# Performance work log

Hardware: AMD Instinct MI355X
Metric: run time of the kernel (lower is better)

Reference implementation:

```python
import jax, jax.numpy as jnp
import numpy as np

WIN = 11      # window_size
SIGMA = 1.5
CH = 1        # channel
LEVELS = 5
C1 = 0.01 ** 2
C2 = 0.03 ** 2
MS_WEIGHTS = np.array([0.0448, 0.2856, 0.3001, 0.2363, 0.1333], dtype=np.float32)


def _gaussian_window(dtype):
    x = jnp.arange(WIN, dtype=jnp.float32) - WIN // 2
    g = jnp.exp(-(x ** 2) / (2.0 * SIGMA ** 2))
    g = g / g.sum()
    w2 = jnp.outer(g, g)  # [K, K]
    # depthwise kernel [C, 1, K, K]
    return jnp.broadcast_to(w2[None, None], (CH, 1, WIN, WIN)).astype(dtype)


def _blur(x, w):
    # depthwise 11x11 Gaussian blur, SAME padding (= pad window_size//2)
    return jax.lax.conv_general_dilated(
        x, w, window_strides=(1, 1), padding='SAME',
        dimension_numbers=('NCHW', 'OIHW', 'NCHW'),
        feature_group_count=CH)


def _ssim_level(img1, img2, w):
    mu1 = _blur(img1, w)
    mu2 = _blur(img2, w)
    mu1_sq = mu1 * mu1
    mu2_sq = mu2 * mu2
    mu1_mu2 = mu1 * mu2
    sigma1_sq = _blur(img1 * img1, w) - mu1_sq
    sigma2_sq = _blur(img2 * img2, w) - mu2_sq
    sigma12 = _blur(img1 * img2, w) - mu1_mu2
    denom_c = sigma1_sq + sigma2_sq + C2
    mcs_map = (2.0 * sigma12 + C2) / denom_c
    ssim_map = ((2.0 * mu1_mu2 + C1) / (mu1_sq + mu2_sq + C1)) * mcs_map
    return ssim_map.mean(), mcs_map.mean()


def _avg_pool2(x):
    B, C, H, W = x.shape
    return x.reshape(B, C, H // 2, 2, W // 2, 2).mean(axis=(3, 5))


def reference(img1, img2):
    w = _gaussian_window(img1.dtype)
    weights = jnp.asarray(MS_WEIGHTS, dtype=img1.dtype)
    mssim, mcs = [], []
    for _ in range(LEVELS):  # small fixed loop over pyramid levels
        s, m = _ssim_level(img1, img2, w)
        mssim.append(s)
        mcs.append(m)
        img1 = _avg_pool2(img1)
        img2 = _avg_pool2(img2)
    mssim = jnp.stack(mssim)
    mcs = jnp.stack(mcs)
    return jnp.prod(mcs[:LEVELS - 1] ** weights[:LEVELS - 1]) * mssim[LEVELS - 1] ** weights[LEVELS - 1]


def setup_inputs() -> dict:
    key = jax.random.key(0)
    k1, k2 = jax.random.split(key)
    img1 = jax.random.uniform(k1, (32, 1, 512, 512), dtype=jnp.float32)
    # correlated second image so ssim/mcs means stay positive (fractional powers)
    img2 = jnp.clip(img1 + 0.1 * jax.random.normal(k2, img1.shape, dtype=jnp.float32), 0.0, 1.0)
    return {"img1": img1, "img2": img2}
```

## Files before the change

### kernel.cpp

```cpp
#include <hip/hip_runtime.h>
#include <math.h>


typedef float v2f __attribute__((ext_vector_type(2)));

#define TILE 32
#define HALO 5
#define SROWS 42
#define SMEM_FLOATS 5384

struct GaussW { float w[11]; };

#define C1_ (0.01f * 0.01f)
#define C2_ (0.03f * 0.03f)

__device__ __forceinline__ void ssim_tile(
        const float* __restrict__ p1, const float* __restrict__ p2,
        int W, int tile_x, int tile_y, const GaussW& gw,
        float2* __restrict__ resslot, float* smem, int tid) {
    v2f* hbSD = (v2f*)smem;
    v2f* hbSQ = (v2f*)(smem + 2 * SROWS * TILE);
    float* red = smem + 4 * SROWS * TILE;

    const bool xfast = (tile_x >= 8) && (tile_x + TILE + 8 <= W);

    for (int it = tid; it < SROWS * 8; it += 256) {
        int r = it >> 3, c4 = it & 7;
        int gy = tile_y + r - HALO;
        int gx0 = tile_x + (c4 << 2) - 8;
        bool rowok = (gy >= 0) && (gy < W);
        const float* row1 = p1 + (size_t)gy * W;
        const float* row2 = p2 + (size_t)gy * W;
        float a1[20], a2[20];
#pragma unroll
        for (int i = 0; i < 20; i++) { a1[i] = 0.f; a2[i] = 0.f; }
        if (xfast) {
            if (rowok) {
#pragma unroll
                for (int q = 0; q < 5; q++) {
                    float4 v1 = *(const float4*)(row1 + gx0 + q * 4);
                    float4 v2v = *(const float4*)(row2 + gx0 + q * 4);
                    a1[q*4+0] = v1.x;  a1[q*4+1] = v1.y;  a1[q*4+2] = v1.z;  a1[q*4+3] = v1.w;
                    a2[q*4+0] = v2v.x; a2[q*4+1] = v2v.y; a2[q*4+2] = v2v.z; a2[q*4+3] = v2v.w;
                }
            }
        } else {
#pragma unroll
            for (int q = 0; q < 5; q++) {
                int g = gx0 + q * 4;
                if (rowok && g >= 0 && g + 4 <= W) {
                    float4 v1 = *(const float4*)(row1 + g);
                    float4 v2v = *(const float4*)(row2 + g);
                    a1[q*4+0] = v1.x;  a1[q*4+1] = v1.y;  a1[q*4+2] = v1.z;  a1[q*4+3] = v1.w;
                    a2[q*4+0] = v2v.x; a2[q*4+1] = v2v.y; a2[q*4+2] = v2v.z; a2[q*4+3] = v2v.w;
                }
            }
        }
        v2f SD[14], SQ[14];
#pragma unroll
        for (int i = 0; i < 14; i++) {
            float x = a1[i + 3], y = a2[i + 3];
            v2f sd = {x + y, x - y};
            SD[i] = sd;
            SQ[i] = sd * sd;
        }
        v2f hsd[4] = {(v2f)(0.f), (v2f)(0.f), (v2f)(0.f), (v2f)(0.f)};
        v2f hsq[4] = {(v2f)(0.f), (v2f)(0.f), (v2f)(0.f), (v2f)(0.f)};
#pragma unroll
        for (int k = 0; k < 11; k++) {
            float wk = gw.w[k];
#pragma unroll
            for (int j = 0; j < 4; j++) {
                hsd[j] += wk * SD[j + k];
                hsq[j] += wk * SQ[j + k];
            }
        }
        int ob = r * TILE + (c4 << 2);
#pragma unroll
        for (int j = 0; j < 4; j++) { hbSD[ob + j] = hsd[j]; hbSQ[ob + j] = hsq[j]; }
    }
    __syncthreads();

    float ssim_v = 0.f, mcs_v = 0.f;
    {
        int tx = tid & 31, y0 = (tid >> 5) * 4;
        v2f msd[4], msq[4];
        {
            v2f v[14];
#pragma unroll
            for (int r = 0; r < 14; r++) v[r] = hbSD[(y0 + r) * TILE + tx];
#pragma unroll
            for (int j = 0; j < 4; j++) {
                v2f s = (v2f)(0.f);
#pragma unroll
                for (int k = 0; k < 11; k++) s += gw.w[k] * v[j + k];
                msd[j] = s;
            }
        }
        {
            v2f v[14];
#pragma unroll
            for (int r = 0; r < 14; r++) v[r] = hbSQ[(y0 + r) * TILE + tx];
#pragma unroll
            for (int j = 0; j < 4; j++) {
                v2f s = (v2f)(0.f);
#pragma unroll
                for (int k = 0; k < 11; k++) s += gw.w[k] * v[j + k];
                msq[j] = s;
            }
        }
#pragma unroll
        for (int j = 0; j < 4; j++) {
            float bs = msd[j].x, bd = msd[j].y;
            float bs2 = msq[j].x, bd2 = msq[j].y;
            float qp = bs * bs, qm = bd * bd;
            float u = bs2 - qp;
            float v = bd2 - qm;
            float mcs  = (0.5f * (u - v) + C2_) / (0.5f * (u + v) + C2_);
            float ssim = ((0.5f * (qp - qm) + C1_) / (0.5f * (qp + qm) + C1_)) * mcs;
            ssim_v += ssim;
            mcs_v  += mcs;
        }
    }

#pragma unroll
    for (int off = 32; off > 0; off >>= 1) {
        ssim_v += __shfl_down(ssim_v, off);
        mcs_v  += __shfl_down(mcs_v, off);
    }
    int wave = tid >> 6, lane = tid & 63;
    if (lane == 0) { red[wave] = ssim_v; red[4 + wave] = mcs_v; }
    __syncthreads();
    if (tid == 0) {
        float S = red[0] + red[1] + red[2] + red[3];
        float M = red[4] + red[5] + red[6] + red[7];
        *resslot = make_float2(S, M);
    }
}

__device__ __forceinline__ void pyramid_region(
        const float* __restrict__ in1, const float* __restrict__ in2,
        int n, int reg,
        float* __restrict__ l1a, float* __restrict__ l1b,
        float* __restrict__ l2a, float* __restrict__ l2b,
        float* __restrict__ l3a, float* __restrict__ l3b,
        float* __restrict__ l4a, float* __restrict__ l4b,
        float* smem, int tid) {
    float* b1 = smem;
    float* b2 = smem + 1024;
    float* c1 = smem + 2048;
    float* c2 = smem + 2304;
    float* d1 = smem + 2560;
    float* d2 = smem + 2624;
    const int rx = reg & 7, ry = reg >> 3;
    const float* p1 = in1 + (size_t)n * 512 * 512;
    const float* p2 = in2 + (size_t)n * 512 * 512;

    for (int i = tid; i < 32 * 16; i += 256) {
        int oy = i >> 4, oxp = i & 15;
        int gy = ry * 64 + 2 * oy, gx = rx * 64 + 4 * oxp;
        float4 r10 = *(const float4*)(p1 + (size_t)gy * 512 + gx);
        float4 r11 = *(const float4*)(p1 + (size_t)(gy + 1) * 512 + gx);
        float4 r20 = *(const float4*)(p2 + (size_t)gy * 512 + gx);
        float4 r21 = *(const float4*)(p2 + (size_t)(gy + 1) * 512 + gx);
        float2 o1 = make_float2(0.25f * (r10.x + r10.y + r11.x + r11.y),
                                0.25f * (r10.z + r10.w + r11.z + r11.w));
        float2 o2 = make_float2(0.25f * (r20.x + r20.y + r21.x + r21.y),
                                0.25f * (r20.z + r20.w + r21.z + r21.w));
        *(float2*)&b1[oy * 32 + 2 * oxp] = o1;
        *(float2*)&b2[oy * 32 + 2 * oxp] = o2;
        size_t o = (size_t)n * 256 * 256 + (size_t)(ry * 32 + oy) * 256 + rx * 32 + 2 * oxp;
        *(float2*)&l1a[o] = o1;
        *(float2*)&l1b[o] = o2;
    }
    __syncthreads();
    if (tid < 16 * 8) {
        int oy = tid >> 3, oxp = tid & 7;
        float4 r10 = *(const float4*)&b1[(2 * oy) * 32 + 4 * oxp];
        float4 r11 = *(const float4*)&b1[(2 * oy + 1) * 32 + 4 * oxp];
        float4 r20 = *(const float4*)&b2[(2 * oy) * 32 + 4 * oxp];
        float4 r21 = *(const float4*)&b2[(2 * oy + 1) * 32 + 4 * oxp];
        float2 o1 = make_float2(0.25f * (r10.x + r10.y + r11.x + r11.y),
                                0.25f * (r10.z + r10.w + r11.z + r11.w));
        float2 o2 = make_float2(0.25f * (r20.x + r20.y + r21.x + r21.y),
                                0.25f * (r20.z + r20.w + r21.z + r21.w));
        *(float2*)&c1[oy * 16 + 2 * oxp] = o1;
        *(float2*)&c2[oy * 16 + 2 * oxp] = o2;
        size_t o = (size_t)n * 128 * 128 + (size_t)(ry * 16 + oy) * 128 + rx * 16 + 2 * oxp;
        *(float2*)&l2a[o] = o1;
        *(float2*)&l2b[o] = o2;
    }
    __syncthreads();
    if (tid < 8 * 4) {
        int oy = tid >> 2, oxp = tid & 3;
        float4 r10 = *(const float4*)&c1[(2 * oy) * 16 + 4 * oxp];
        float4 r11 = *(const float4*)&c1[(2 * oy + 1) * 16 + 4 * oxp];
        float4 r20 = *(const float4*)&c2[(2 * oy) * 16 + 4 * oxp];
        float4 r21 = *(const float4*)&c2[(2 * oy + 1) * 16 + 4 * oxp];
        float2 o1 = make_float2(0.25f * (r10.x + r10.y + r11.x + r11.y),
                                0.25f * (r10.z + r10.w + r11.z + r11.w));
        float2 o2 = make_float2(0.25f * (r20.x + r20.y + r21.x + r21.y),
                                0.25f * (r20.z + r20.w + r21.z + r21.w));
        *(float2*)&d1[oy * 8 + 2 * oxp] = o1;
        *(float2*)&d2[oy * 8 + 2 * oxp] = o2;
        size_t o = (size_t)n * 64 * 64 + (size_t)(ry * 8 + oy) * 64 + rx * 8 + 2 * oxp;
        *(float2*)&l3a[o] = o1;
        *(float2*)&l3b[o] = o2;
    }
    __syncthreads();
    if (tid < 4 * 2) {
        int oy = tid >> 1, oxp = tid & 1;
        float4 r10 = *(const float4*)&d1[(2 * oy) * 8 + 4 * oxp];
        float4 r11 = *(const float4*)&d1[(2 * oy + 1) * 8 + 4 * oxp];
        float4 r20 = *(const float4*)&d2[(2 * oy) * 8 + 4 * oxp];
        float4 r21 = *(const float4*)&d2[(2 * oy + 1) * 8 + 4 * oxp];
        float2 o1 = make_float2(0.25f * (r10.x + r10.y + r11.x + r11.y),
                                0.25f * (r10.z + r10.w + r11.z + r11.w));
        float2 o2 = make_float2(0.25f * (r20.x + r20.y + r21.x + r21.y),
                                0.25f * (r20.z + r20.w + r21.z + r21.w));
        size_t o = (size_t)n * 32 * 32 + (size_t)(ry * 4 + oy) * 32 + rx * 4 + 2 * oxp;
        *(float2*)&l4a[o] = o1;
        *(float2*)&l4b[o] = o2;
    }
}

__global__ __launch_bounds__(256, 7) void d1_kernel(
        const float* __restrict__ i0a, const float* __restrict__ i0b,
        float* __restrict__ l1a, float* __restrict__ l1b,
        float* __restrict__ l2a, float* __restrict__ l2b,
        float* __restrict__ l3a, float* __restrict__ l3b,
        float* __restrict__ l4a, float* __restrict__ l4b,
        float2* __restrict__ res0, GaussW gw) {
    __shared__ float smem[SMEM_FLOATS];
    const int tid = threadIdx.x;
    const int t = blockIdx.x;
    const int n = blockIdx.y;
    if (t < 64) {
        pyramid_region(i0a, i0b, n, t, l1a, l1b, l2a, l2b, l3a, l3b, l4a, l4b,
                       smem, tid);
    } else {
        int idx = t - 64;
        const float* p1 = i0a + (size_t)n * 512 * 512;
        const float* p2 = i0b + (size_t)n * 512 * 512;
        ssim_tile(p1, p2, 512, (idx & 15) << 5, (idx >> 4) << 5,
                  gw, &res0[n * 256 + idx], smem, tid);
    }
}

__global__ __launch_bounds__(256, 7) void d2_kernel(
        const float* __restrict__ l1a, const float* __restrict__ l1b,
        const float* __restrict__ l2a, const float* __restrict__ l2b,
        const float* __restrict__ l3a, const float* __restrict__ l3b,
        const float* __restrict__ l4a, const float* __restrict__ l4b,
        float2* __restrict__ res1, float2* __restrict__ res2,
        float2* __restrict__ res3, float2* __restrict__ res4, GaussW gw) {
    __shared__ float smem[SMEM_FLOATS];
    const int tid = threadIdx.x;
    const int t = blockIdx.x;
    const int n = blockIdx.y;
    const float* b1;
    const float* b2;
    int W, tx, ty;
    float2* slot;
    if (t < 64)      { W = 256; b1 = l1a; b2 = l1b; tx = (t & 7) << 5; ty = (t >> 3) << 5; slot = &res1[n * 64 + t]; }
    else if (t < 80) { int i = t - 64; W = 128; b1 = l2a; b2 = l2b; tx = (i & 3) << 5; ty = (i >> 2) << 5; slot = &res2[n * 16 + i]; }
    else if (t < 84) { int i = t - 80; W = 64; b1 = l3a; b2 = l3b; tx = (i & 1) << 5; ty = (i >> 1) << 5; slot = &res3[n * 4 + i]; }
    else             { W = 32; b1 = l4a; b2 = l4b; tx = 0; ty = 0; slot = &res4[n]; }
    ssim_tile(b1 + (size_t)n * W * W, b2 + (size_t)n * W * W, W,
              tx, ty, gw, slot, smem, tid);
}

__global__ void finalize_kernel(const float2* __restrict__ res0,
                                const float2* __restrict__ res1,
                                const float2* __restrict__ res2,
                                const float2* __restrict__ res3,
                                const float2* __restrict__ res4,
                                float* __restrict__ out, int N) {
    __shared__ float2 redf[5][4];
    const int tid = threadIdx.x;
    const float2* rr[5] = {res0, res1, res2, res3, res4};
    const int cnts[5] = {N * 256, N * 64, N * 16, N * 4, N};
#pragma unroll
    for (int l = 0; l < 5; l++) {
        float sx = 0.f, sy = 0.f;
        for (int i = tid; i < cnts[l]; i += 256) {
            float2 v = rr[l][i];
            sx += v.x;
            sy += v.y;
        }
#pragma unroll
        for (int off = 32; off > 0; off >>= 1) {
            sx += __shfl_down(sx, off);
            sy += __shfl_down(sy, off);
        }
        if ((tid & 63) == 0) redf[l][tid >> 6] = make_float2(sx, sy);
    }
    __syncthreads();
    if (tid == 0) {
        const float wts[5] = {0.0448f, 0.2856f, 0.3001f, 0.2363f, 0.1333f};
        float r = 1.f;
#pragma unroll
        for (int l = 0; l < 5; l++) {
            float sx = redf[l][0].x + redf[l][1].x + redf[l][2].x + redf[l][3].x;
            float sy = redf[l][0].y + redf[l][1].y + redf[l][2].y + redf[l][3].y;
            int Hl = 512 >> l;
            float cnt = (float)N * (float)Hl * (float)Hl;
            float ssim_m = sx / cnt;
            float mcs_m  = sy / cnt;
            if (l < 4) r *= powf(mcs_m, wts[l]);
            else       r *= powf(ssim_m, wts[4]);
        }
        out[0] = r;
    }
}

extern "C" void kernel_launch(void* const* d_in, const int* in_sizes, int n_in,
                              void* d_out, int out_size, void* d_ws, size_t ws_size,
                              hipStream_t stream) {
    const float* img1 = (const float*)d_in[0];
    const float* img2 = (const float*)d_in[1];
    float* out = (float*)d_out;
    const int HW0 = 512 * 512;
    const int N = in_sizes[0] / HW0;

    float* base = (float*)d_ws;
    size_t cur = 0;
    float* l1a = base + cur; cur += (size_t)N * 256 * 256;
    float* l1b = base + cur; cur += (size_t)N * 256 * 256;
    float* l2a = base + cur; cur += (size_t)N * 128 * 128;
    float* l2b = base + cur; cur += (size_t)N * 128 * 128;
    float* l3a = base + cur; cur += (size_t)N * 64 * 64;
    float* l3b = base + cur; cur += (size_t)N * 64 * 64;
    float* l4a = base + cur; cur += (size_t)N * 32 * 32;
    float* l4b = base + cur; cur += (size_t)N * 32 * 32;
    float2* res0 = (float2*)(base + cur); cur += (size_t)N * 512;
    float2* res1 = (float2*)(base + cur); cur += (size_t)N * 128;
    float2* res2 = (float2*)(base + cur); cur += (size_t)N * 32;
    float2* res3 = (float2*)(base + cur); cur += (size_t)N * 8;
    float2* res4 = (float2*)(base + cur); cur += (size_t)N * 2;

    GaussW gw;
    {
        double g[11], sum = 0.0;
        for (int i = 0; i < 11; i++) {
            double x = (double)(i - 5);
            g[i] = exp(-(x * x) / (2.0 * 1.5 * 1.5));
            sum += g[i];
        }
        for (int i = 0; i < 11; i++) gw.w[i] = (float)(g[i] / sum);
    }

    d1_kernel<<<dim3(320, N), 256, 0, stream>>>(
        img1, img2, l1a, l1b, l2a, l2b, l3a, l3b, l4a, l4b, res0, gw);
    d2_kernel<<<dim3(85, N), 256, 0, stream>>>(
        l1a, l1b, l2a, l2b, l3a, l3b, l4a, l4b, res1, res2, res3, res4, gw);
    finalize_kernel<<<1, 256, 0, stream>>>(res0, res1, res2, res3, res4, out, N);
}
```

Before: 156.0 us.

## Fuse pyramid downsampling into SSIM tile blocks using wave shuffles

Removes the 64 dedicated pyramid-building blocks per image. Each SSIM tile block now computes the 2x2 pooled pyramid levels 1-4 for its own 32x32 tile before the SSIM work. It uses a Morton-ordered thread mapping and wave-level shuffle reductions in place of shared-memory staging and block barriers. This cuts the grid from 320 to 256 blocks per image and reuses the tile's inputs, which are likely cached, for the pooling. The cost is extra uncoalesced float2 loads, and scattered small stores for the coarser levels.

Measured after the change: 162.1 us. +3.9%, slower.

```diff
diff --git a/kernel.cpp b/kernel.cpp
--- a/kernel.cpp
+++ b/kernel.cpp
@@ -138,92 +138,6 @@
     }
 }
 
-__device__ __forceinline__ void pyramid_region(
-        const float* __restrict__ in1, const float* __restrict__ in2,
-        int n, int reg,
-        float* __restrict__ l1a, float* __restrict__ l1b,
-        float* __restrict__ l2a, float* __restrict__ l2b,
-        float* __restrict__ l3a, float* __restrict__ l3b,
-        float* __restrict__ l4a, float* __restrict__ l4b,
-        float* smem, int tid) {
-    float* b1 = smem;
-    float* b2 = smem + 1024;
-    float* c1 = smem + 2048;
-    float* c2 = smem + 2304;
-    float* d1 = smem + 2560;
-    float* d2 = smem + 2624;
-    const int rx = reg & 7, ry = reg >> 3;
-    const float* p1 = in1 + (size_t)n * 512 * 512;
-    const float* p2 = in2 + (size_t)n * 512 * 512;
-
-    for (int i = tid; i < 32 * 16; i += 256) {
-        int oy = i >> 4, oxp = i & 15;
-        int gy = ry * 64 + 2 * oy, gx = rx * 64 + 4 * oxp;
-        float4 r10 = *(const float4*)(p1 + (size_t)gy * 512 + gx);
-        float4 r11 = *(const float4*)(p1 + (size_t)(gy + 1) * 512 + gx);
-        float4 r20 = *(const float4*)(p2 + (size_t)gy * 512 + gx);
-        float4 r21 = *(const float4*)(p2 + (size_t)(gy + 1) * 512 + gx);
-        float2 o1 = make_float2(0.25f * (r10.x + r10.y + r11.x + r11.y),
-                                0.25f * (r10.z + r10.w + r11.z + r11.w));
-        float2 o2 = make_float2(0.25f * (r20.x + r20.y + r21.x + r21.y),
-                                0.25f * (r20.z + r20.w + r21.z + r21.w));
-        *(float2*)&b1[oy * 32 + 2 * oxp] = o1;
-        *(float2*)&b2[oy * 32 + 2 * oxp] = o2;
-        size_t o = (size_t)n * 256 * 256 + (size_t)(ry * 32 + oy) * 256 + rx * 32 + 2 * oxp;
-        *(float2*)&l1a[o] = o1;
-        *(float2*)&l1b[o] = o2;
-    }
-    __syncthreads();
-    if (tid < 16 * 8) {
-        int oy = tid >> 3, oxp = tid & 7;
-        float4 r10 = *(const float4*)&b1[(2 * oy) * 32 + 4 * oxp];
-        float4 r11 = *(const float4*)&b1[(2 * oy + 1) * 32 + 4 * oxp];
-        float4 r20 = *(const float4*)&b2[(2 * oy) * 32 + 4 * oxp];
-        float4 r21 = *(const float4*)&b2[(2 * oy + 1) * 32 + 4 * oxp];
-        float2 o1 = make_float2(0.25f * (r10.x + r10.y + r11.x + r11.y),
-                                0.25f * (r10.z + r10.w + r11.z + r11.w));
-        float2 o2 = make_float2(0.25f * (r20.x + r20.y + r21.x + r21.y),
-                                0.25f * (r20.z + r20.w + r21.z + r21.w));
-        *(float2*)&c1[oy * 16 + 2 * oxp] = o1;
-        *(float2*)&c2[oy * 16 + 2 * oxp] = o2;
-        size_t o = (size_t)n * 128 * 128 + (size_t)(ry * 16 + oy) * 128 + rx * 16 + 2 * oxp;
-        *(float2*)&l2a[o] = o1;
-        *(float2*)&l2b[o] = o2;
-    }
-    __syncthreads();
-    if (tid < 8 * 4) {
-        int oy = tid >> 2, oxp = tid & 3;
-        float4 r10 = *(const float4*)&c1[(2 * oy) * 16 + 4 * oxp];
-        float4 r11 = *(const float4*)&c1[(2 * oy + 1) * 16 + 4 * oxp];
-        float4 r20 = *(const float4*)&c2[(2 * oy) * 16 + 4 * oxp];
-        float4 r21 = *(const float4*)&c2[(2 * oy + 1) * 16 + 4 * oxp];
-        float2 o1 = make_float2(0.25f * (r10.x + r10.y + r11.x + r11.y),
-                                0.25f * (r10.z + r10.w + r11.z + r11.w));
-        float2 o2 = make_float2(0.25f * (r20.x + r20.y + r21.x + r21.y),
-                                0.25f * (r20.z + r20.w + r21.z + r21.w));
-        *(float2*)&d1[oy * 8 + 2 * oxp] = o1;
-        *(float2*)&d2[oy * 8 + 2 * oxp] = o2;
-        size_t o = (size_t)n * 64 * 64 + (size_t)(ry * 8 + oy) * 64 + rx * 8 + 2 * oxp;
-        *(float2*)&l3a[o] = o1;
-        *(float2*)&l3b[o] = o2;
-    }
-    __syncthreads();
-    if (tid < 4 * 2) {
-        int oy = tid >> 1, oxp = tid & 1;
-        float4 r10 = *(const float4*)&d1[(2 * oy) * 8 + 4 * oxp];
-        float4 r11 = *(const float4*)&d1[(2 * oy + 1) * 8 + 4 * oxp];
-        float4 r20 = *(const float4*)&d2[(2 * oy) * 8 + 4 * oxp];
-        float4 r21 = *(const float4*)&d2[(2 * oy + 1) * 8 + 4 * oxp];
-        float2 o1 = make_float2(0.25f * (r10.x + r10.y + r11.x + r11.y),
-                                0.25f * (r10.z + r10.w + r11.z + r11.w));
-        float2 o2 = make_float2(0.25f * (r20.x + r20.y + r21.x + r21.y),
-                                0.25f * (r20.z + r20.w + r21.z + r21.w));
-        size_t o = (size_t)n * 32 * 32 + (size_t)(ry * 4 + oy) * 32 + rx * 4 + 2 * oxp;
-        *(float2*)&l4a[o] = o1;
-        *(float2*)&l4b[o] = o2;
-    }
-}
-
 __global__ __launch_bounds__(256, 7) void d1_kernel(
         const float* __restrict__ i0a, const float* __restrict__ i0b,
         float* __restrict__ l1a, float* __restrict__ l1b,
@@ -233,18 +147,51 @@
         float2* __restrict__ res0, GaussW gw) {
     __shared__ float smem[SMEM_FLOATS];
     const int tid = threadIdx.x;
-    const int t = blockIdx.x;
+    const int idx = blockIdx.x;
     const int n = blockIdx.y;
-    if (t < 64) {
-        pyramid_region(i0a, i0b, n, t, l1a, l1b, l2a, l2b, l3a, l3b, l4a, l4b,
-                       smem, tid);
-    } else {
-        int idx = t - 64;
-        const float* p1 = i0a + (size_t)n * 512 * 512;
-        const float* p2 = i0b + (size_t)n * 512 * 512;
-        ssim_tile(p1, p2, 512, (idx & 15) << 5, (idx >> 4) << 5,
-                  gw, &res0[n * 256 + idx], smem, tid);
-    }
+    const int tile_x = (idx & 15) << 5;
+    const int tile_y = (idx >> 4) << 5;
+    const float* p1 = i0a + (size_t)n * 512 * 512;
+    const float* p2 = i0b + (size_t)n * 512 * 512;
+
+    {
+        int px = ((tid >> 0) & 1) | ((tid >> 1) & 2) | ((tid >> 2) & 4) | ((tid >> 3) & 8);
+        int py = ((tid >> 1) & 1) | ((tid >> 2) & 2) | ((tid >> 3) & 4) | ((tid >> 4) & 8);
+        int gx = tile_x + 2 * px, gy = tile_y + 2 * py;
+        float2 u0 = *(const float2*)(p1 + (size_t)gy * 512 + gx);
+        float2 u1 = *(const float2*)(p1 + (size_t)(gy + 1) * 512 + gx);
+        float2 w0 = *(const float2*)(p2 + (size_t)gy * 512 + gx);
+        float2 w1 = *(const float2*)(p2 + (size_t)(gy + 1) * 512 + gx);
+        float va = 0.25f * ((u0.x + u0.y) + (u1.x + u1.y));
+        float vb = 0.25f * ((w0.x + w0.y) + (w1.x + w1.y));
+        int b1x = (tile_x >> 1) + px, b1y = (tile_y >> 1) + py;
+        l1a[(size_t)n * 256 * 256 + (size_t)b1y * 256 + b1x] = va;
+        l1b[(size_t)n * 256 * 256 + (size_t)b1y * 256 + b1x] = vb;
+        float sa = va, sb = vb;
+        sa += __shfl_xor(sa, 1);  sb += __shfl_xor(sb, 1);
+        sa += __shfl_xor(sa, 2);  sb += __shfl_xor(sb, 2);
+        if ((tid & 3) == 0) {
+            int x = (tile_x >> 2) + (px >> 1), y = (tile_y >> 2) + (py >> 1);
+            l2a[(size_t)n * 128 * 128 + (size_t)y * 128 + x] = 0.25f * sa;
+            l2b[(size_t)n * 128 * 128 + (size_t)y * 128 + x] = 0.25f * sb;
+        }
+        sa += __shfl_xor(sa, 4);  sb += __shfl_xor(sb, 4);
+        sa += __shfl_xor(sa, 8);  sb += __shfl_xor(sb, 8);
+        if ((tid & 15) == 0) {
+            int x = (tile_x >> 3) + (px >> 2), y = (tile_y >> 3) + (py >> 2);
+            l3a[(size_t)n * 64 * 64 + (size_t)y * 64 + x] = 0.0625f * sa;
+            l3b[(size_t)n * 64 * 64 + (size_t)y * 64 + x] = 0.0625f * sb;
+        }
+        sa += __shfl_xor(sa, 16); sb += __shfl_xor(sb, 16);
+        sa += __shfl_xor(sa, 32); sb += __shfl_xor(sb, 32);
+        if ((tid & 63) == 0) {
+            int x = (tile_x >> 4) + (px >> 3), y = (tile_y >> 4) + (py >> 3);
+            l4a[(size_t)n * 32 * 32 + (size_t)y * 32 + x] = 0.015625f * sa;
+            l4b[(size_t)n * 32 * 32 + (size_t)y * 32 + x] = 0.015625f * sb;
+        }
+    }
+
+    ssim_tile(p1, p2, 512, tile_x, tile_y, gw, &res0[n * 256 + idx], smem, tid);
 }
 
 __global__ __launch_bounds__(256, 7) void d2_kernel(
@@ -350,7 +297,7 @@
         for (int i = 0; i < 11; i++) gw.w[i] = (float)(g[i] / sum);
     }
 
-    d1_kernel<<<dim3(320, N), 256, 0, stream>>>(
+    d1_kernel<<<dim3(256, N), 256, 0, stream>>>(
         img1, img2, l1a, l1b, l2a, l2b, l3a, l3b, l4a, l4b, res0, gw);
     d2_kernel<<<dim3(85, N), 256, 0, stream>>>(
         l1a, l1b, l2a, l2b, l3a, l3b, l4a, l4b, res1, res2, res3, res4, gw);
```
